# Performance work log

Hardware: AMD Instinct MI355X
Metric: run time of the kernel (lower is better)

## Reference

```python
import jax, jax.numpy as jnp
import numpy as np

OBS_DIM, GOAL_DIM, NUM_SKILLS, ACTION_DIM = 256, 64, 16, 32
HIDDEN = 128
BATCH = 65536


def setup_inputs() -> dict:
    key = jax.random.key(0)
    ks = jax.random.split(key, 10)
    s = lambda k, shape, fan_in: jax.random.normal(k, shape, jnp.float32) * (1.0 / np.sqrt(fan_in))
    return {
        "obs": jax.random.normal(ks[0], (BATCH, OBS_DIM), jnp.float32),
        "goals": jax.random.normal(ks[1], (BATCH, GOAL_DIM), jnp.float32),
        # gate (AlphaNet) params
        "Wa1": s(ks[2], (OBS_DIM + GOAL_DIM, HIDDEN), OBS_DIM + GOAL_DIM),
        "ba1": jnp.zeros((HIDDEN,), jnp.float32),
        "Wa2": s(ks[3], (HIDDEN, NUM_SKILLS), HIDDEN),
        "ba2": jnp.zeros((NUM_SKILLS,), jnp.float32),
        # stacked executor params: [S, in, out]
        "W1": s(ks[4], (NUM_SKILLS, OBS_DIM, HIDDEN), OBS_DIM),
        "b1": jnp.zeros((NUM_SKILLS, HIDDEN), jnp.float32),
        "W2": s(ks[5], (NUM_SKILLS, HIDDEN, ACTION_DIM), HIDDEN),
        "b2": jnp.zeros((NUM_SKILLS, ACTION_DIM), jnp.float32),
    }


def reference(obs, goals, Wa1, ba1, Wa2, ba2, W1, b1, W2, b2):
    # gate: softmax(Linear(ReLU(Linear(cat(obs, goals)))))
    concat_input = jnp.concatenate([obs, goals], axis=-1)  # [B, O+G]
    ha = jax.nn.relu(concat_input @ Wa1 + ba1)             # [B, H]
    alphas = jax.nn.softmax(ha @ Wa2 + ba2, axis=-1)       # [B, S]

    # all experts as one grouped GEMM over stacked weights
    h = jax.nn.relu(jnp.einsum("bo,soh->bsh", obs, W1) + b1[None])  # [B, S, H]
    skill_outputs = jnp.einsum("bsh,sha->bsa", h, W2) + b2[None]    # [B, S, A]

    # weighted sum over skills
    mixed_action = jnp.einsum("bsa,bs->ba", skill_outputs, alphas)  # [B, A]
    return mixed_action, alphas
```

## Files before the change

### kernel.cpp

```cpp
#include <hip/hip_runtime.h>


typedef __attribute__((ext_vector_type(8))) short    bf16x8;
typedef __attribute__((ext_vector_type(4))) float    f32x4;
typedef __attribute__((ext_vector_type(4))) _Float16 f16x4;

#define GATE_W1_OFF   0
#define GATE_W2_OFF   81920
#define SKILL_OFF     86016
#define SKILL_STRIDE  73728
#define SKILL_W2_OFF  65536
#define LDS_BYTES     159744

__device__ __forceinline__ unsigned short f2bf(float f) {
  unsigned u = __builtin_bit_cast(unsigned, f);
  return (unsigned short)((u + 0x7FFFu + ((u >> 16) & 1u)) >> 16);
}

__device__ __forceinline__ bf16x8 pack_bf8(f32x4 a, f32x4 b) {
  bf16x8 r;
  r[0] = (short)f2bf(a[0]); r[1] = (short)f2bf(a[1]);
  r[2] = (short)f2bf(a[2]); r[3] = (short)f2bf(a[3]);
  r[4] = (short)f2bf(b[0]); r[5] = (short)f2bf(b[1]);
  r[6] = (short)f2bf(b[2]); r[7] = (short)f2bf(b[3]);
  return r;
}

__global__ void prep_weights(const float* __restrict__ Wa1, const float* __restrict__ Wa2,
                             const float* __restrict__ W1,  const float* __restrict__ W2,
                             unsigned char* __restrict__ ws) {
  int i = blockIdx.x * 256 + threadIdx.x;
  if (i < 524288) {
    int s = i >> 15, r = i & 32767, h = r >> 8, o = r & 255;
    float v = W1[(s * 256 + o) * 128 + h];
    *(unsigned short*)(ws + SKILL_OFF + s * SKILL_STRIDE + h * 512 +
                       ((2 * o) ^ ((h & 7) << 4))) = f2bf(v);
  } else if (i < 589824) {
    int j = i - 524288, s = j >> 12, r = j & 4095, a = r >> 7, h = r & 127;
    float v = W2[(s * 128 + h) * 32 + a];
    *(_Float16*)(ws + SKILL_OFF + s * SKILL_STRIDE + SKILL_W2_OFF + a * 256 +
                 ((2 * h) ^ ((a & 7) << 3))) = (_Float16)v;
  } else if (i < 630784) {
    int j = i - 589824, h = j / 320, o = j - h * 320;
    float v = Wa1[o * 128 + h];
    *(unsigned short*)(ws + GATE_W1_OFF + h * 640 +
                       ((2 * o) ^ ((h & 7) << 4))) = f2bf(v);
  } else if (i < 632832) {
    int j = i - 630784, n = j >> 7, h = j & 127;
    float v = Wa2[h * 16 + n];
    *(_Float16*)(ws + GATE_W2_OFF + n * 256 +
                 ((2 * h) ^ ((n & 7) << 3))) = (_Float16)v;
  }
}

__device__ __forceinline__ void stage_lin(const unsigned char* gsrc, unsigned char* ldst,
                                          int tid, int bytes) {
  for (int off = tid * 16; off < bytes; off += 512 * 16) {
    __builtin_amdgcn_global_load_lds(
        (const __attribute__((address_space(1))) unsigned int*)(const void*)(gsrc + off),
        (__attribute__((address_space(3))) unsigned int*)(void*)(ldst + off), 16, 0, 0);
  }
}

__global__ __launch_bounds__(512, 2)
void mop_fused(const float* __restrict__ obs, const float* __restrict__ goals,
               const float* __restrict__ ba1, const float* __restrict__ ba2,
               const float* __restrict__ b1,  const float* __restrict__ b2,
               const unsigned char* __restrict__ ws, float* __restrict__ dout) {
  extern __shared__ unsigned char smem[];
  const int tid  = threadIdx.x;
  const int lane = tid & 63;
  const int wave = tid >> 6;
  const int l15  = lane & 15;
  const int g    = lane >> 4;
  const int swz4 = (lane & 7) << 4;
  const int swz3 = (lane & 7) << 3;
  const int rowbase = blockIdx.x * 256 + wave * 32;

  float* out_mixed = dout;
  float* out_alpha = dout + 65536 * 32;

  stage_lin(ws, smem, tid, LDS_BYTES);

  bf16x8 obsf[2][8];
  bf16x8 goalf[2][2];
  #pragma unroll
  for (int nb = 0; nb < 2; ++nb) {
    const float* rp = obs + (size_t)(rowbase + nb * 16 + l15) * 256 + 8 * g;
    #pragma unroll
    for (int t = 0; t < 8; ++t) {
      f32x4 a = *(const f32x4*)(rp + 32 * t);
      f32x4 c = *(const f32x4*)(rp + 32 * t + 4);
      obsf[nb][t] = pack_bf8(a, c);
    }
    const float* gp = goals + (size_t)(rowbase + nb * 16 + l15) * 64 + 8 * g;
    #pragma unroll
    for (int t = 0; t < 2; ++t) {
      f32x4 a = *(const f32x4*)(gp + 32 * t);
      f32x4 c = *(const f32x4*)(gp + 32 * t + 4);
      goalf[nb][t] = pack_bf8(a, c);
    }
  }

  __syncthreads();

  f32x4 gacc[2][8];
  #pragma unroll
  for (int ht = 0; ht < 8; ++ht) {
    f32x4 bias = *(const f32x4*)(ba1 + 16 * ht + 4 * g);
    gacc[0][ht] = bias; gacc[1][ht] = bias;
  }
  #pragma unroll
  for (int t = 0; t < 10; ++t) {
    bf16x8 bf0 = (t < 8) ? obsf[0][t] : goalf[0][t - 8];
    bf16x8 bf1 = (t < 8) ? obsf[1][t] : goalf[1][t - 8];
    #pragma unroll
    for (int ht = 0; ht < 8; ++ht) {
      int row = 16 * ht + l15;
      bf16x8 af = *(const bf16x8*)(smem + GATE_W1_OFF + row * 640 +
                                   ((64 * t + 16 * g) ^ swz4));
      gacc[0][ht] = __builtin_amdgcn_mfma_f32_16x16x32_bf16(af, bf0, gacc[0][ht], 0, 0, 0);
      gacc[1][ht] = __builtin_amdgcn_mfma_f32_16x16x32_bf16(af, bf1, gacc[1][ht], 0, 0, 0);
    }
  }

  f32x4 alph[2];
  #pragma unroll
  for (int nb = 0; nb < 2; ++nb) {
    f32x4 lacc = *(const f32x4*)(ba2 + 4 * g);
    #pragma unroll
    for (int ht = 0; ht < 8; ++ht) {
      f32x4 v = gacc[nb][ht];
      f16x4 hf;
      hf[0] = (_Float16)fmaxf(v[0], 0.f); hf[1] = (_Float16)fmaxf(v[1], 0.f);
      hf[2] = (_Float16)fmaxf(v[2], 0.f); hf[3] = (_Float16)fmaxf(v[3], 0.f);
      f16x4 wf = *(const f16x4*)(smem + GATE_W2_OFF + l15 * 256 +
                                 ((32 * ht + 8 * g) ^ swz3));
      lacc = __builtin_amdgcn_mfma_f32_16x16x16f16(wf, hf, lacc, 0, 0, 0);
    }
    float m = fmaxf(fmaxf(lacc[0], lacc[1]), fmaxf(lacc[2], lacc[3]));
    m = fmaxf(m, __shfl_xor(m, 16, 64));
    m = fmaxf(m, __shfl_xor(m, 32, 64));
    f32x4 e;
    e[0] = __expf(lacc[0] - m); e[1] = __expf(lacc[1] - m);
    e[2] = __expf(lacc[2] - m); e[3] = __expf(lacc[3] - m);
    float ssum = e[0] + e[1] + e[2] + e[3];
    ssum += __shfl_xor(ssum, 16, 64);
    ssum += __shfl_xor(ssum, 32, 64);
    float inv = 1.0f / ssum;
    alph[nb] = e * inv;
    *(f32x4*)(out_alpha + (size_t)(rowbase + nb * 16 + l15) * 16 + 4 * g) = alph[nb];
  }

  __syncthreads();

  f32x4 macc[2][2] = {};
  for (int s = 0; s < 16; ++s) {
    const unsigned char* buf = smem + ((s & 1) ? 0 : SKILL_OFF);
    if (s < 15) {
      unsigned char* nbuf = smem + (((s + 1) & 1) ? 0 : SKILL_OFF);
      stage_lin(ws + SKILL_OFF + (size_t)(s + 1) * SKILL_STRIDE, nbuf, tid, SKILL_STRIDE);
    }
    const int asrc = ((s >> 2) << 4) | l15;
    float p0 = (s & 1) ? alph[0][1] : alph[0][0];
    float p1 = (s & 1) ? alph[0][3] : alph[0][2];
    float as0 = __shfl((s & 2) ? p1 : p0, asrc, 64);
    float q0 = (s & 1) ? alph[1][1] : alph[1][0];
    float q1 = (s & 1) ? alph[1][3] : alph[1][2];
    float as1 = __shfl((s & 2) ? q1 : q0, asrc, 64);

    #pragma unroll
    for (int ht = 0; ht < 8; ++ht) {
      f32x4 bias = *(const f32x4*)(b1 + s * 128 + 16 * ht + 4 * g);
      f32x4 acc0 = bias, acc1 = bias;
      #pragma unroll
      for (int t = 0; t < 8; ++t) {
        int row = 16 * ht + l15;
        bf16x8 af = *(const bf16x8*)(buf + row * 512 + ((64 * t + 16 * g) ^ swz4));
        acc0 = __builtin_amdgcn_mfma_f32_16x16x32_bf16(af, obsf[0][t], acc0, 0, 0, 0);
        acc1 = __builtin_amdgcn_mfma_f32_16x16x32_bf16(af, obsf[1][t], acc1, 0, 0, 0);
      }
      f16x4 hf0, hf1;
      hf0[0] = (_Float16)(fmaxf(acc0[0], 0.f) * as0);
      hf0[1] = (_Float16)(fmaxf(acc0[1], 0.f) * as0);
      hf0[2] = (_Float16)(fmaxf(acc0[2], 0.f) * as0);
      hf0[3] = (_Float16)(fmaxf(acc0[3], 0.f) * as0);
      hf1[0] = (_Float16)(fmaxf(acc1[0], 0.f) * as1);
      hf1[1] = (_Float16)(fmaxf(acc1[1], 0.f) * as1);
      hf1[2] = (_Float16)(fmaxf(acc1[2], 0.f) * as1);
      hf1[3] = (_Float16)(fmaxf(acc1[3], 0.f) * as1);
      #pragma unroll
      for (int ta = 0; ta < 2; ++ta) {
        f16x4 wf = *(const f16x4*)(buf + SKILL_W2_OFF + (16 * ta + l15) * 256 +
                                   ((32 * ht + 8 * g) ^ swz3));
        macc[0][ta] = __builtin_amdgcn_mfma_f32_16x16x16f16(wf, hf0, macc[0][ta], 0, 0, 0);
        macc[1][ta] = __builtin_amdgcn_mfma_f32_16x16x16f16(wf, hf1, macc[1][ta], 0, 0, 0);
      }
    }
    #pragma unroll
    for (int ta = 0; ta < 2; ++ta) {
      f32x4 b2v = *(const f32x4*)(b2 + s * 32 + 16 * ta + 4 * g);
      macc[0][ta] = macc[0][ta] + b2v * as0;
      macc[1][ta] = macc[1][ta] + b2v * as1;
    }
    __syncthreads();
  }

  #pragma unroll
  for (int nb = 0; nb < 2; ++nb) {
    #pragma unroll
    for (int ta = 0; ta < 2; ++ta) {
      *(f32x4*)(out_mixed + (size_t)(rowbase + nb * 16 + l15) * 32 + 16 * ta + 4 * g) =
          macc[nb][ta];
    }
  }
}

extern "C" void kernel_launch(void* const* d_in, const int* in_sizes, int n_in,
                              void* d_out, int out_size, void* d_ws, size_t ws_size,
                              hipStream_t stream) {
  const float* obs   = (const float*)d_in[0];
  const float* goals = (const float*)d_in[1];
  const float* Wa1   = (const float*)d_in[2];
  const float* ba1   = (const float*)d_in[3];
  const float* Wa2   = (const float*)d_in[4];
  const float* ba2   = (const float*)d_in[5];
  const float* W1    = (const float*)d_in[6];
  const float* b1    = (const float*)d_in[7];
  const float* W2    = (const float*)d_in[8];
  const float* b2    = (const float*)d_in[9];
  unsigned char* ws  = (unsigned char*)d_ws;
  float* out = (float*)d_out;

  prep_weights<<<2472, 256, 0, stream>>>(Wa1, Wa2, W1, W2, ws);
  mop_fused<<<256, 512, LDS_BYTES, stream>>>(obs, goals, ba1, ba2, b1, b2, ws, out);
}
```

Baseline: 102.8 us.

## Pad skill weight LDS layout, overlap first skill load with gate, pack f16 epilogue

Skill weights now use a padded row-stride layout in LDS instead of the XOR-swizzled one, so per-lane base addresses are computed once and inner loads use constant offsets. Only the gate weights are staged before the gate GEMM; the first skill's weights are loaded during gate compute instead of up front. The ReLU/alpha-scale epilogue uses packed f16 conversion and max, bias loads are hoisted out of the inner loop, and wave priority is raised around the MFMA section. Round-toward-zero f16 conversion slightly changes rounding, and the padded layout uses somewhat more LDS.

```diff
diff --git a/kernel.cpp b/kernel.cpp
--- a/kernel.cpp
+++ b/kernel.cpp
@@ -7,10 +7,13 @@
 
 #define GATE_W1_OFF   0
 #define GATE_W2_OFF   81920
+#define GATE_BYTES    86016
+#define S_W1_STRIDE   528
+#define S_W2_OFF      67584
+#define S_W2_STRIDE   264
+#define S_IMG         76032
 #define SKILL_OFF     86016
-#define SKILL_STRIDE  73728
-#define SKILL_W2_OFF  65536
-#define LDS_BYTES     159744
+#define LDS_BYTES     162048
 
 __device__ __forceinline__ unsigned short f2bf(float f) {
   unsigned u = __builtin_bit_cast(unsigned, f);
@@ -26,6 +29,16 @@
   return r;
 }
 
+#define RELU_SCALE_PACK(dst, v, av, z)                                   \
+  {                                                                      \
+    auto lo_ = __builtin_amdgcn_cvt_pkrtz((v)[0], (v)[1]);               \
+    auto hi_ = __builtin_amdgcn_cvt_pkrtz((v)[2], (v)[3]);               \
+    lo_ = __builtin_elementwise_max(lo_, z) * (av);                      \
+    hi_ = __builtin_elementwise_max(hi_, z) * (av);                      \
+    dst[0] = (_Float16)lo_[0]; dst[1] = (_Float16)lo_[1];                \
+    dst[2] = (_Float16)hi_[0]; dst[3] = (_Float16)hi_[1];                \
+  }
+
 __global__ void prep_weights(const float* __restrict__ Wa1, const float* __restrict__ Wa2,
                              const float* __restrict__ W1,  const float* __restrict__ W2,
                              unsigned char* __restrict__ ws) {
@@ -33,13 +46,12 @@
   if (i < 524288) {
     int s = i >> 15, r = i & 32767, h = r >> 8, o = r & 255;
     float v = W1[(s * 256 + o) * 128 + h];
-    *(unsigned short*)(ws + SKILL_OFF + s * SKILL_STRIDE + h * 512 +
-                       ((2 * o) ^ ((h & 7) << 4))) = f2bf(v);
+    *(unsigned short*)(ws + SKILL_OFF + s * S_IMG + h * S_W1_STRIDE + 2 * o) = f2bf(v);
   } else if (i < 589824) {
     int j = i - 524288, s = j >> 12, r = j & 4095, a = r >> 7, h = r & 127;
     float v = W2[(s * 128 + h) * 32 + a];
-    *(_Float16*)(ws + SKILL_OFF + s * SKILL_STRIDE + SKILL_W2_OFF + a * 256 +
-                 ((2 * h) ^ ((a & 7) << 3))) = (_Float16)v;
+    *(_Float16*)(ws + SKILL_OFF + s * S_IMG + S_W2_OFF + a * S_W2_STRIDE + 2 * h) =
+        (_Float16)v;
   } else if (i < 630784) {
     int j = i - 589824, h = j / 320, o = j - h * 320;
     float v = Wa1[o * 128 + h];
@@ -80,7 +92,10 @@
   float* out_mixed = dout;
   float* out_alpha = dout + 65536 * 32;
 
-  stage_lin(ws, smem, tid, LDS_BYTES);
+  const int lw1 = l15 * S_W1_STRIDE + 16 * g;
+  const int lw2 = S_W2_OFF + l15 * S_W2_STRIDE + 8 * g;
+
+  stage_lin(ws, smem, tid, GATE_BYTES);
 
   bf16x8 obsf[2][8];
   bf16x8 goalf[2][2];
@@ -103,6 +118,8 @@
   }
 
   __syncthreads();
+
+  stage_lin(ws + SKILL_OFF, smem + GATE_BYTES, tid, S_IMG);
 
   f32x4 gacc[2][8];
   #pragma unroll
@@ -124,6 +141,7 @@
     }
   }
 
+  const auto zh = __builtin_amdgcn_cvt_pkrtz(0.f, 0.f);
   f32x4 alph[2];
   #pragma unroll
   for (int nb = 0; nb < 2; ++nb) {
@@ -132,8 +150,14 @@
     for (int ht = 0; ht < 8; ++ht) {
       f32x4 v = gacc[nb][ht];
       f16x4 hf;
-      hf[0] = (_Float16)fmaxf(v[0], 0.f); hf[1] = (_Float16)fmaxf(v[1], 0.f);
-      hf[2] = (_Float16)fmaxf(v[2], 0.f); hf[3] = (_Float16)fmaxf(v[3], 0.f);
+      {
+        auto lo_ = __builtin_amdgcn_cvt_pkrtz(v[0], v[1]);
+        auto hi_ = __builtin_amdgcn_cvt_pkrtz(v[2], v[3]);
+        lo_ = __builtin_elementwise_max(lo_, zh);
+        hi_ = __builtin_elementwise_max(hi_, zh);
+        hf[0] = (_Float16)lo_[0]; hf[1] = (_Float16)lo_[1];
+        hf[2] = (_Float16)hi_[0]; hf[3] = (_Float16)hi_[1];
+      }
       f16x4 wf = *(const f16x4*)(smem + GATE_W2_OFF + l15 * 256 +
                                  ((32 * ht + 8 * g) ^ swz3));
       lacc = __builtin_amdgcn_mfma_f32_16x16x16f16(wf, hf, lacc, 0, 0, 0);
@@ -156,10 +180,10 @@
 
   f32x4 macc[2][2] = {};
   for (int s = 0; s < 16; ++s) {
-    const unsigned char* buf = smem + ((s & 1) ? 0 : SKILL_OFF);
+    const unsigned char* buf = smem + ((s & 1) ? 0 : GATE_BYTES);
     if (s < 15) {
-      unsigned char* nbuf = smem + (((s + 1) & 1) ? 0 : SKILL_OFF);
-      stage_lin(ws + SKILL_OFF + (size_t)(s + 1) * SKILL_STRIDE, nbuf, tid, SKILL_STRIDE);
+      unsigned char* nbuf = smem + (((s + 1) & 1) ? 0 : GATE_BYTES);
+      stage_lin(ws + SKILL_OFF + (size_t)(s + 1) * S_IMG, nbuf, tid, S_IMG);
     }
     const int asrc = ((s >> 2) << 4) | l15;
     float p0 = (s & 1) ? alph[0][1] : alph[0][0];
@@ -168,40 +192,46 @@
     float q0 = (s & 1) ? alph[1][1] : alph[1][0];
     float q1 = (s & 1) ? alph[1][3] : alph[1][2];
     float as1 = __shfl((s & 2) ? q1 : q0, asrc, 64);
-
+    const auto a0h = __builtin_amdgcn_cvt_pkrtz(as0, as0);
+    const auto a1h = __builtin_amdgcn_cvt_pkrtz(as1, as1);
+
+    f32x4 b1v[8];
+    #pragma unroll
+    for (int ht = 0; ht < 8; ++ht)
+      b1v[ht] = *(const f32x4*)(b1 + s * 128 + 16 * ht + 4 * g);
+    f32x4 b2v[2];
+    #pragma unroll
+    for (int ta = 0; ta < 2; ++ta)
+      b2v[ta] = *(const f32x4*)(b2 + s * 32 + 16 * ta + 4 * g);
+
+    const unsigned char* w1p = buf + lw1;
+    const unsigned char* w2p = buf + lw2;
+
+    __builtin_amdgcn_s_setprio(1);
     #pragma unroll
     for (int ht = 0; ht < 8; ++ht) {
-      f32x4 bias = *(const f32x4*)(b1 + s * 128 + 16 * ht + 4 * g);
-      f32x4 acc0 = bias, acc1 = bias;
+      f32x4 acc0 = b1v[ht], acc1 = b1v[ht];
       #pragma unroll
       for (int t = 0; t < 8; ++t) {
-        int row = 16 * ht + l15;
-        bf16x8 af = *(const bf16x8*)(buf + row * 512 + ((64 * t + 16 * g) ^ swz4));
+        bf16x8 af = *(const bf16x8*)(w1p + ht * 8448 + t * 64);
         acc0 = __builtin_amdgcn_mfma_f32_16x16x32_bf16(af, obsf[0][t], acc0, 0, 0, 0);
         acc1 = __builtin_amdgcn_mfma_f32_16x16x32_bf16(af, obsf[1][t], acc1, 0, 0, 0);
       }
       f16x4 hf0, hf1;
-      hf0[0] = (_Float16)(fmaxf(acc0[0], 0.f) * as0);
-      hf0[1] = (_Float16)(fmaxf(acc0[1], 0.f) * as0);
-      hf0[2] = (_Float16)(fmaxf(acc0[2], 0.f) * as0);
-      hf0[3] = (_Float16)(fmaxf(acc0[3], 0.f) * as0);
-      hf1[0] = (_Float16)(fmaxf(acc1[0], 0.f) * as1);
-      hf1[1] = (_Float16)(fmaxf(acc1[1], 0.f) * as1);
-      hf1[2] = (_Float16)(fmaxf(acc1[2], 0.f) * as1);
-      hf1[3] = (_Float16)(fmaxf(acc1[3], 0.f) * as1);
+      RELU_SCALE_PACK(hf0, acc0, a0h, zh);
+      RELU_SCALE_PACK(hf1, acc1, a1h, zh);
       #pragma unroll
       for (int ta = 0; ta < 2; ++ta) {
-        f16x4 wf = *(const f16x4*)(buf + SKILL_W2_OFF + (16 * ta + l15) * 256 +
-                                   ((32 * ht + 8 * g) ^ swz3));
+        f16x4 wf = *(const f16x4*)(w2p + ta * 4224 + ht * 32);
         macc[0][ta] = __builtin_amdgcn_mfma_f32_16x16x16f16(wf, hf0, macc[0][ta], 0, 0, 0);
         macc[1][ta] = __builtin_amdgcn_mfma_f32_16x16x16f16(wf, hf1, macc[1][ta], 0, 0, 0);
       }
     }
+    __builtin_amdgcn_s_setprio(0);
     #pragma unroll
     for (int ta = 0; ta < 2; ++ta) {
-      f32x4 b2v = *(const f32x4*)(b2 + s * 32 + 16 * ta + 4 * g);
-      macc[0][ta] = macc[0][ta] + b2v * as0;
-      macc[1][ta] = macc[1][ta] + b2v * as1;
+      macc[0][ta] = macc[0][ta] + b2v[ta] * as0;
+      macc[1][ta] = macc[1][ta] + b2v[ta] * as1;
     }
     __syncthreads();
   }
```

Measured after the change: 99.33 us. 3.3% less time.
